# Kernel tuning notes

Hardware: AMD Instinct MI355X
Metric: run time of the kernel (lower is better)

The kernel has to match this reference:

```python
import jax, jax.numpy as jnp
import numpy as np

NB, NSITES, N_NGB, DIM, NG = 32, 65536, 13, 3, 48


def setup_inputs() -> dict:
    key = jax.random.key(0)
    k1, k2, k3, k4, k5 = jax.random.split(key, 5)
    In = jax.random.normal(k1, (NB, 1, NSITES), dtype=jnp.float32)
    # wtVC ~ Normal(mean=1.0, std=0.1), size (dim, N_ngb)
    wtVC = 1.0 + 0.1 * jax.random.normal(k2, (DIM, N_NGB), dtype=jnp.float32)
    # gdiags: (Ng*dim, Ng*dim) symmetry-rotation mixing matrix
    gdiags = jax.random.normal(k3, (NG * DIM, NG * DIM), dtype=jnp.float32)
    GnnPerms = jax.random.randint(k4, (NG, N_NGB), 0, N_NGB)
    NNsites = jax.random.randint(k5, (N_NGB, NSITES), 0, NSITES)
    return {"In": In, "wtVC": wtVC, "gdiags": gdiags,
            "GnnPerms": GnnPerms, "NNsites": NNsites}


def reference(In, wtVC, gdiags, GnnPerms, NNsites):
    Ng = GnnPerms.shape[0]
    dim, n_ngb = wtVC.shape
    # RotateParams: row g*dim+d of the permuted weight is wtVC[d, GnnPerms[g]]
    Wp = wtVC[:, GnnPerms]                              # [dim, Ng, N_ngb]
    Wp = jnp.transpose(Wp, (1, 0, 2)).reshape(Ng * dim, n_ngb)
    Wt = gdiags @ Wp                                    # [Ng*dim, N_ngb]
    # Final op in torch is sum over g / Ng; fold that into the weight to
    # avoid materializing the [Nb, Ng*dim, Nsites] intermediate.
    Wmean = Wt.reshape(Ng, dim, n_ngb).mean(axis=0)     # [dim, N_ngb]
    # RearrangeInput: gathered[b, j, s] = In[b, 0, NNsites[j, s]]
    gathered = In[:, 0, :][:, NNsites]                  # [Nb, N_ngb, Nsites]
    # out[b, d, s] = sum_j Wmean[d, j] * gathered[b, j, s]
    return jnp.einsum('dj,bjs->bds', Wmean, gathered)   # [Nb, dim, Nsites]
```

## Files before the change

kernel.cpp:

```cpp
#include <hip/hip_runtime.h>

#define NB_     32
#define NSITES_ 65536
#define NNGB_   13
#define DIM_    3
#define NG_     48
#define GD_     (NG_ * DIM_)

typedef unsigned uvec4_t __attribute__((ext_vector_type(4)));

__global__ __launch_bounds__(256) void prep_kernel_78486(
    const float* __restrict__ In,
    const float* __restrict__ wtVC,
    const float* __restrict__ gdiags,
    const int*   __restrict__ perms,
    float*  __restrict__ wm,
    ushort* __restrict__ InT,
    int nTransBlocks)
{
    const int t = threadIdx.x;
    if ((int)blockIdx.x < DIM_ * NNGB_) {
        const int p = blockIdx.x;
        const int d = p / NNGB_, j = p - NNGB_ * d;
        __shared__ float wpj[GD_];
        __shared__ float red[4];
        if (t < GD_) {
            int g = t / DIM_, dp = t - DIM_ * g;
            wpj[t] = wtVC[dp * NNGB_ + perms[g * NNGB_ + j]];
        }
        __syncthreads();
        float acc = 0.f;
        for (int e = t; e < NG_ * GD_; e += 256) {
            int g = e / GD_;
            int k = e - g * GD_;
            acc += gdiags[(g * DIM_ + d) * GD_ + k] * wpj[k];
        }
#pragma unroll
        for (int off = 32; off > 0; off >>= 1) acc += __shfl_down(acc, off, 64);
        if ((t & 63) == 0) red[t >> 6] = acc;
        __syncthreads();
        if (t == 0) wm[p] = (red[0] + red[1] + red[2] + red[3]) * (1.0f / NG_);
    } else {
        const int tb = blockIdx.x - DIM_ * NNGB_;
        if (tb >= nTransBlocks) return;
        const int s0 = tb * 64;
        __shared__ ushort tile[64][40];
        const int sl = t & 63, bq = t >> 6;
#pragma unroll
        for (int r = 0; r < 8; r++) {
            int b = bq * 8 + r;
            float v = __builtin_nontemporal_load(&In[b * NSITES_ + s0 + sl]);
            unsigned fu = __float_as_uint(v);
            fu = fu + 0x7FFFu + ((fu >> 16) & 1u);
            tile[sl][b] = (ushort)(fu >> 16);
        }
        __syncthreads();
        const int site = t >> 2, q = t & 3;
        uvec4_t val = *(const uvec4_t*)&tile[site][q * 8];
        *(uvec4_t*)(InT + (size_t)(s0 + site) * NB_ + q * 8) = val;
    }
}

__global__ __launch_bounds__(256) void gather_kernel_78486(
    const ushort* __restrict__ InT,
    const int*    __restrict__ nn,
    const float*  __restrict__ wm,
    float* __restrict__ out)
{
    const int t = blockIdx.x * 256 + threadIdx.x;
    const int h = t & 1;
    const int s = t >> 1;

    __shared__ float ws[DIM_ * NNGB_];
    if (threadIdx.x < DIM_ * NNGB_) ws[threadIdx.x] = wm[threadIdx.x];
    __syncthreads();

    float acc0[16], acc1[16], acc2[16];
#pragma unroll
    for (int i = 0; i < 16; i++) { acc0[i] = 0.f; acc1[i] = 0.f; acc2[i] = 0.f; }

#pragma unroll
    for (int j = 0; j < NNGB_; j++) {
        int idx = __builtin_nontemporal_load(&nn[j * NSITES_ + s]);
        const uvec4_t* p = (const uvec4_t*)(InT + ((size_t)idx << 5) + (h << 4));
        uvec4_t a = p[0];
        uvec4_t b = p[1];
        unsigned uu[8] = {a.x, a.y, a.z, a.w, b.x, b.y, b.z, b.w};
        float v[16];
#pragma unroll
        for (int k = 0; k < 8; k++) {
            v[2 * k]     = __uint_as_float(uu[k] << 16);
            v[2 * k + 1] = __uint_as_float(uu[k] & 0xFFFF0000u);
        }
        float w0 = ws[j], w1 = ws[NNGB_ + j], w2 = ws[2 * NNGB_ + j];
#pragma unroll
        for (int i = 0; i < 16; i++) {
            acc0[i] += w0 * v[i];
            acc1[i] += w1 * v[i];
            acc2[i] += w2 * v[i];
        }
    }

#pragma unroll
    for (int i = 0; i < 16; i++) {
        int b = h * 16 + i;
        size_t base = (size_t)b * DIM_ * NSITES_ + s;
        __builtin_nontemporal_store(acc0[i], &out[base]);
        __builtin_nontemporal_store(acc1[i], &out[base + NSITES_]);
        __builtin_nontemporal_store(acc2[i], &out[base + 2 * NSITES_]);
    }
}

__global__ __launch_bounds__(256) void gather_fallback_78486(
    const float* __restrict__ In,
    const int*   __restrict__ nn,
    const float* __restrict__ wm,
    float* __restrict__ out)
{
    const int t = blockIdx.x * 256 + threadIdx.x;
    const int s = t & (NSITES_ - 1);
    const int b = t >> 16;
    float a0 = 0.f, a1 = 0.f, a2 = 0.f;
#pragma unroll
    for (int j = 0; j < NNGB_; j++) {
        int idx = nn[j * NSITES_ + s];
        float v = In[b * NSITES_ + idx];
        a0 += wm[0 * NNGB_ + j] * v;
        a1 += wm[1 * NNGB_ + j] * v;
        a2 += wm[2 * NNGB_ + j] * v;
    }
    out[(b * DIM_ + 0) * NSITES_ + s] = a0;
    out[(b * DIM_ + 1) * NSITES_ + s] = a1;
    out[(b * DIM_ + 2) * NSITES_ + s] = a2;
}

extern "C" void kernel_launch(void* const* d_in, const int* in_sizes, int n_in,
                              void* d_out, int out_size, void* d_ws, size_t ws_size,
                              hipStream_t stream)
{
    const float* In     = (const float*)d_in[0];
    const float* wtVC   = (const float*)d_in[1];
    const float* gdiags = (const float*)d_in[2];
    const int*   perms  = (const int*)d_in[3];
    const int*   nn     = (const int*)d_in[4];
    float* out = (float*)d_out;

    float*  wm  = (float*)d_ws;
    ushort* InT = (ushort*)((char*)d_ws + 1024);

    const size_t need = 1024 + (size_t)NSITES_ * NB_ * sizeof(ushort);
    const int nTrans = NSITES_ / 64;

    if (ws_size >= need) {
        prep_kernel_78486<<<DIM_ * NNGB_ + nTrans, 256, 0, stream>>>(
            In, wtVC, gdiags, perms, wm, InT, nTrans);
        gather_kernel_78486<<<(NSITES_ * 2) / 256, 256, 0, stream>>>(
            InT, nn, wm, out);
    } else {
        prep_kernel_78486<<<DIM_ * NNGB_, 256, 0, stream>>>(
            In, wtVC, gdiags, perms, wm, (ushort*)nullptr, 0);
        gather_fallback_78486<<<(NSITES_ * NB_) / 256, 256, 0, stream>>>(
            In, nn, wm, out);
    }
}
```

Baseline: 99.11 us.

## Fuse prep and gather into one cooperative kernel with grid sync

Merges the weight-reduction/bf16-transpose prep kernel and the gather kernel into a single cooperative launch of 1024 blocks that synchronizes the whole grid between the phases, which removes one kernel launch and the gap between them. The gather now gives each site 4 threads handling 8 batches apiece instead of 2 threads with 16, and the nontemporal load/store hints are dropped. A cooperative launch requires all 1024 blocks to be co-resident (launch_bounds 256,4). If that launch fails, the code falls back to the two-kernel path with the new 4-thread gather mapping.

```diff
diff --git a/kernel.cpp b/kernel.cpp
--- a/kernel.cpp
+++ b/kernel.cpp
@@ -1,4 +1,7 @@
 #include <hip/hip_runtime.h>
+#include <hip/hip_cooperative_groups.h>
+
+namespace cg = cooperative_groups;
 
 #define NB_     32
 #define NSITES_ 65536
@@ -8,6 +11,103 @@
 #define GD_     (NG_ * DIM_)
 
 typedef unsigned uvec4_t __attribute__((ext_vector_type(4)));
+
+__global__ __launch_bounds__(256, 4) void fused_kernel_78486(
+    const float* __restrict__ In,
+    const float* __restrict__ wtVC,
+    const float* __restrict__ gdiags,
+    const int*   __restrict__ perms,
+    const int*   __restrict__ nn,
+    float*  __restrict__ wm,
+    ushort* __restrict__ InT,
+    float*  __restrict__ out)
+{
+    const int t   = threadIdx.x;
+    const int blk = blockIdx.x;
+
+    __shared__ ushort tile[64][40];
+    __shared__ float  wpj[GD_];
+    __shared__ float  red[4];
+    __shared__ float  ws[DIM_ * NNGB_];
+
+    const int s0 = blk * 64;
+    const int sl = t & 63, bq = t >> 6;
+#pragma unroll
+    for (int r = 0; r < 8; r++) {
+        int b = bq * 8 + r;
+        float v = In[b * NSITES_ + s0 + sl];
+        unsigned fu = __float_as_uint(v);
+        fu = fu + 0x7FFFu + ((fu >> 16) & 1u);
+        tile[sl][b] = (ushort)(fu >> 16);
+    }
+    __syncthreads();
+    {
+        const int site = t >> 2, q = t & 3;
+        uvec4_t val = *(const uvec4_t*)&tile[site][q * 8];
+        *(uvec4_t*)(InT + (size_t)(s0 + site) * NB_ + q * 8) = val;
+    }
+
+    if (blk < DIM_ * NNGB_) {
+        const int d = blk / NNGB_, j = blk - NNGB_ * d;
+        if (t < GD_) {
+            int g = t / DIM_, dp = t - DIM_ * g;
+            wpj[t] = wtVC[dp * NNGB_ + perms[g * NNGB_ + j]];
+        }
+        __syncthreads();
+        float acc = 0.f;
+        for (int e = t; e < NG_ * GD_; e += 256) {
+            int g = e / GD_;
+            int k = e - g * GD_;
+            acc += gdiags[(g * DIM_ + d) * GD_ + k] * wpj[k];
+        }
+#pragma unroll
+        for (int off = 32; off > 0; off >>= 1) acc += __shfl_down(acc, off, 64);
+        if ((t & 63) == 0) red[t >> 6] = acc;
+        __syncthreads();
+        if (t == 0) wm[blk] = (red[0] + red[1] + red[2] + red[3]) * (1.0f / NG_);
+    }
+
+    cg::this_grid().sync();
+
+    if (t < DIM_ * NNGB_) ws[t] = wm[t];
+    __syncthreads();
+
+    const int s = blk * 64 + (t >> 2);
+    const int q = t & 3;
+
+    float a0[8], a1[8], a2[8];
+#pragma unroll
+    for (int i = 0; i < 8; i++) { a0[i] = 0.f; a1[i] = 0.f; a2[i] = 0.f; }
+
+#pragma unroll
+    for (int j = 0; j < NNGB_; j++) {
+        int idx = nn[j * NSITES_ + s];
+        uvec4_t u = *(const uvec4_t*)(InT + ((size_t)idx << 5) + (q << 3));
+        unsigned uu[4] = {u.x, u.y, u.z, u.w};
+        float v[8];
+#pragma unroll
+        for (int k = 0; k < 4; k++) {
+            v[2 * k]     = __uint_as_float(uu[k] << 16);
+            v[2 * k + 1] = __uint_as_float(uu[k] & 0xFFFF0000u);
+        }
+        float w0 = ws[j], w1 = ws[NNGB_ + j], w2 = ws[2 * NNGB_ + j];
+#pragma unroll
+        for (int i = 0; i < 8; i++) {
+            a0[i] += w0 * v[i];
+            a1[i] += w1 * v[i];
+            a2[i] += w2 * v[i];
+        }
+    }
+
+#pragma unroll
+    for (int i = 0; i < 8; i++) {
+        int b = q * 8 + i;
+        size_t base = (size_t)b * DIM_ * NSITES_ + s;
+        out[base]               = a0[i];
+        out[base + NSITES_]     = a1[i];
+        out[base + 2 * NSITES_] = a2[i];
+    }
+}
 
 __global__ __launch_bounds__(256) void prep_kernel_78486(
     const float* __restrict__ In,
@@ -49,7 +149,7 @@
 #pragma unroll
         for (int r = 0; r < 8; r++) {
             int b = bq * 8 + r;
-            float v = __builtin_nontemporal_load(&In[b * NSITES_ + s0 + sl]);
+            float v = In[b * NSITES_ + s0 + sl];
             unsigned fu = __float_as_uint(v);
             fu = fu + 0x7FFFu + ((fu >> 16) & 1u);
             tile[sl][b] = (ushort)(fu >> 16);
@@ -68,46 +168,44 @@
     float* __restrict__ out)
 {
     const int t = blockIdx.x * 256 + threadIdx.x;
-    const int h = t & 1;
-    const int s = t >> 1;
+    const int q = t & 3;
+    const int s = t >> 2;
 
     __shared__ float ws[DIM_ * NNGB_];
     if (threadIdx.x < DIM_ * NNGB_) ws[threadIdx.x] = wm[threadIdx.x];
     __syncthreads();
 
-    float acc0[16], acc1[16], acc2[16];
-#pragma unroll
-    for (int i = 0; i < 16; i++) { acc0[i] = 0.f; acc1[i] = 0.f; acc2[i] = 0.f; }
+    float a0[8], a1[8], a2[8];
+#pragma unroll
+    for (int i = 0; i < 8; i++) { a0[i] = 0.f; a1[i] = 0.f; a2[i] = 0.f; }
 
 #pragma unroll
     for (int j = 0; j < NNGB_; j++) {
-        int idx = __builtin_nontemporal_load(&nn[j * NSITES_ + s]);
-        const uvec4_t* p = (const uvec4_t*)(InT + ((size_t)idx << 5) + (h << 4));
-        uvec4_t a = p[0];
-        uvec4_t b = p[1];
-        unsigned uu[8] = {a.x, a.y, a.z, a.w, b.x, b.y, b.z, b.w};
-        float v[16];
-#pragma unroll
-        for (int k = 0; k < 8; k++) {
+        int idx = nn[j * NSITES_ + s];
+        uvec4_t u = *(const uvec4_t*)(InT + ((size_t)idx << 5) + (q << 3));
+        unsigned uu[4] = {u.x, u.y, u.z, u.w};
+        float v[8];
+#pragma unroll
+        for (int k = 0; k < 4; k++) {
             v[2 * k]     = __uint_as_float(uu[k] << 16);
             v[2 * k + 1] = __uint_as_float(uu[k] & 0xFFFF0000u);
         }
         float w0 = ws[j], w1 = ws[NNGB_ + j], w2 = ws[2 * NNGB_ + j];
 #pragma unroll
-        for (int i = 0; i < 16; i++) {
-            acc0[i] += w0 * v[i];
-            acc1[i] += w1 * v[i];
-            acc2[i] += w2 * v[i];
-        }
-    }
-
-#pragma unroll
-    for (int i = 0; i < 16; i++) {
-        int b = h * 16 + i;
+        for (int i = 0; i < 8; i++) {
+            a0[i] += w0 * v[i];
+            a1[i] += w1 * v[i];
+            a2[i] += w2 * v[i];
+        }
+    }
+
+#pragma unroll
+    for (int i = 0; i < 8; i++) {
+        int b = q * 8 + i;
         size_t base = (size_t)b * DIM_ * NSITES_ + s;
-        __builtin_nontemporal_store(acc0[i], &out[base]);
-        __builtin_nontemporal_store(acc1[i], &out[base + NSITES_]);
-        __builtin_nontemporal_store(acc2[i], &out[base + 2 * NSITES_]);
+        out[base]               = a0[i];
+        out[base + NSITES_]     = a1[i];
+        out[base + 2 * NSITES_] = a2[i];
     }
 }
 
@@ -120,18 +218,18 @@
     const int t = blockIdx.x * 256 + threadIdx.x;
     const int s = t & (NSITES_ - 1);
     const int b = t >> 16;
-    float a0 = 0.f, a1 = 0.f, a2 = 0.f;
+    float x0 = 0.f, x1 = 0.f, x2 = 0.f;
 #pragma unroll
     for (int j = 0; j < NNGB_; j++) {
         int idx = nn[j * NSITES_ + s];
         float v = In[b * NSITES_ + idx];
-        a0 += wm[0 * NNGB_ + j] * v;
-        a1 += wm[1 * NNGB_ + j] * v;
-        a2 += wm[2 * NNGB_ + j] * v;
-    }
-    out[(b * DIM_ + 0) * NSITES_ + s] = a0;
-    out[(b * DIM_ + 1) * NSITES_ + s] = a1;
-    out[(b * DIM_ + 2) * NSITES_ + s] = a2;
+        x0 += wm[0 * NNGB_ + j] * v;
+        x1 += wm[1 * NNGB_ + j] * v;
+        x2 += wm[2 * NNGB_ + j] * v;
+    }
+    out[(b * DIM_ + 0) * NSITES_ + s] = x0;
+    out[(b * DIM_ + 1) * NSITES_ + s] = x1;
+    out[(b * DIM_ + 2) * NSITES_ + s] = x2;
 }
 
 extern "C" void kernel_launch(void* const* d_in, const int* in_sizes, int n_in,
@@ -152,10 +250,17 @@
     const int nTrans = NSITES_ / 64;
 
     if (ws_size >= need) {
-        prep_kernel_78486<<<DIM_ * NNGB_ + nTrans, 256, 0, stream>>>(
-            In, wtVC, gdiags, perms, wm, InT, nTrans);
-        gather_kernel_78486<<<(NSITES_ * 2) / 256, 256, 0, stream>>>(
-            InT, nn, wm, out);
+        void* args[] = {(void*)&In, (void*)&wtVC, (void*)&gdiags, (void*)&perms,
+                        (void*)&nn, (void*)&wm, (void*)&InT, (void*)&out};
+        hipError_t e = hipLaunchCooperativeKernel(
+            (const void*)fused_kernel_78486, dim3(nTrans), dim3(256),
+            args, 0, stream);
+        if (e != hipSuccess) {
+            prep_kernel_78486<<<DIM_ * NNGB_ + nTrans, 256, 0, stream>>>(
+                In, wtVC, gdiags, perms, wm, InT, nTrans);
+            gather_kernel_78486<<<(NSITES_ * 4) / 256, 256, 0, stream>>>(
+                InT, nn, wm, out);
+        }
     } else {
         prep_kernel_78486<<<DIM_ * NNGB_, 256, 0, stream>>>(
             In, wtVC, gdiags, perms, wm, (ushort*)nullptr, 0);
```

Result: slower. 227.2 us (+129.3%).

## Split gather across four threads per site and batch all gathers upfront

Applied to the files above, without the earlier changes.

The gather kernel now gives each site to four threads, each covering 8 batches, instead of two threads covering 16. All 13 neighbour indices and gathered 16-byte vectors are loaded up front for memory-level parallelism. Weights are read straight from global memory instead of staged through shared memory with a barrier. Nontemporal loads and stores are replaced with ordinary ones. Each 64-byte row is now read by four threads, which gives more parallelism and fewer registers per thread. In exchange, each neighbour index is loaded by four threads, and output stores are spread over more threads.

```diff
diff --git a/kernel.cpp b/kernel.cpp
--- a/kernel.cpp
+++ b/kernel.cpp
@@ -49,7 +49,7 @@
 #pragma unroll
         for (int r = 0; r < 8; r++) {
             int b = bq * 8 + r;
-            float v = __builtin_nontemporal_load(&In[b * NSITES_ + s0 + sl]);
+            float v = In[b * NSITES_ + s0 + sl];
             unsigned fu = __float_as_uint(v);
             fu = fu + 0x7FFFu + ((fu >> 16) & 1u);
             tile[sl][b] = (ushort)(fu >> 16);
@@ -68,46 +68,47 @@
     float* __restrict__ out)
 {
     const int t = blockIdx.x * 256 + threadIdx.x;
-    const int h = t & 1;
-    const int s = t >> 1;
+    const int q = t & 3;
+    const int s = t >> 2;
 
-    __shared__ float ws[DIM_ * NNGB_];
-    if (threadIdx.x < DIM_ * NNGB_) ws[threadIdx.x] = wm[threadIdx.x];
-    __syncthreads();
+    int idx[NNGB_];
+#pragma unroll
+    for (int j = 0; j < NNGB_; j++) idx[j] = nn[j * NSITES_ + s];
 
-    float acc0[16], acc1[16], acc2[16];
+    uvec4_t u[NNGB_];
 #pragma unroll
-    for (int i = 0; i < 16; i++) { acc0[i] = 0.f; acc1[i] = 0.f; acc2[i] = 0.f; }
+    for (int j = 0; j < NNGB_; j++)
+        u[j] = *(const uvec4_t*)(InT + ((size_t)idx[j] << 5) + (q << 3));
+
+    float a0[8], a1[8], a2[8];
+#pragma unroll
+    for (int i = 0; i < 8; i++) { a0[i] = 0.f; a1[i] = 0.f; a2[i] = 0.f; }
 
 #pragma unroll
     for (int j = 0; j < NNGB_; j++) {
-        int idx = __builtin_nontemporal_load(&nn[j * NSITES_ + s]);
-        const uvec4_t* p = (const uvec4_t*)(InT + ((size_t)idx << 5) + (h << 4));
-        uvec4_t a = p[0];
-        uvec4_t b = p[1];
-        unsigned uu[8] = {a.x, a.y, a.z, a.w, b.x, b.y, b.z, b.w};
-        float v[16];
+        unsigned uu[4] = {u[j].x, u[j].y, u[j].z, u[j].w};
+        float v[8];
 #pragma unroll
-        for (int k = 0; k < 8; k++) {
+        for (int k = 0; k < 4; k++) {
             v[2 * k]     = __uint_as_float(uu[k] << 16);
             v[2 * k + 1] = __uint_as_float(uu[k] & 0xFFFF0000u);
         }
-        float w0 = ws[j], w1 = ws[NNGB_ + j], w2 = ws[2 * NNGB_ + j];
+        float w0 = wm[j], w1 = wm[NNGB_ + j], w2 = wm[2 * NNGB_ + j];
 #pragma unroll
-        for (int i = 0; i < 16; i++) {
-            acc0[i] += w0 * v[i];
-            acc1[i] += w1 * v[i];
-            acc2[i] += w2 * v[i];
+        for (int i = 0; i < 8; i++) {
+            a0[i] += w0 * v[i];
+            a1[i] += w1 * v[i];
+            a2[i] += w2 * v[i];
         }
     }
 
 #pragma unroll
-    for (int i = 0; i < 16; i++) {
-        int b = h * 16 + i;
+    for (int i = 0; i < 8; i++) {
+        int b = q * 8 + i;
         size_t base = (size_t)b * DIM_ * NSITES_ + s;
-        __builtin_nontemporal_store(acc0[i], &out[base]);
-        __builtin_nontemporal_store(acc1[i], &out[base + NSITES_]);
-        __builtin_nontemporal_store(acc2[i], &out[base + 2 * NSITES_]);
+        out[base]               = a0[i];
+        out[base + NSITES_]     = a1[i];
+        out[base + 2 * NSITES_] = a2[i];
     }
 }
 
@@ -120,18 +121,18 @@
     const int t = blockIdx.x * 256 + threadIdx.x;
     const int s = t & (NSITES_ - 1);
     const int b = t >> 16;
-    float a0 = 0.f, a1 = 0.f, a2 = 0.f;
+    float x0 = 0.f, x1 = 0.f, x2 = 0.f;
 #pragma unroll
     for (int j = 0; j < NNGB_; j++) {
         int idx = nn[j * NSITES_ + s];
         float v = In[b * NSITES_ + idx];
-        a0 += wm[0 * NNGB_ + j] * v;
-        a1 += wm[1 * NNGB_ + j] * v;
-        a2 += wm[2 * NNGB_ + j] * v;
+        x0 += wm[0 * NNGB_ + j] * v;
+        x1 += wm[1 * NNGB_ + j] * v;
+        x2 += wm[2 * NNGB_ + j] * v;
     }
-    out[(b * DIM_ + 0) * NSITES_ + s] = a0;
-    out[(b * DIM_ + 1) * NSITES_ + s] = a1;
-    out[(b * DIM_ + 2) * NSITES_ + s] = a2;
+    out[(b * DIM_ + 0) * NSITES_ + s] = x0;
+    out[(b * DIM_ + 1) * NSITES_ + s] = x1;
+    out[(b * DIM_ + 2) * NSITES_ + s] = x2;
 }
 
 extern "C" void kernel_launch(void* const* d_in, const int* in_sizes, int n_in,
@@ -154,7 +155,7 @@
     if (ws_size >= need) {
         prep_kernel_78486<<<DIM_ * NNGB_ + nTrans, 256, 0, stream>>>(
             In, wtVC, gdiags, perms, wm, InT, nTrans);
-        gather_kernel_78486<<<(NSITES_ * 2) / 256, 256, 0, stream>>>(
+        gather_kernel_78486<<<(NSITES_ * 4) / 256, 256, 0, stream>>>(
             InT, nn, wm, out);
     } else {
         prep_kernel_78486<<<DIM_ * NNGB_, 256, 0, stream>>>(
```

Measured after the change: 93.38 us (median of 2 runs). 1.06x faster.
